# Kernel optimization log

Hardware: AMD Instinct MI355X
Metric: run time of the kernel (lower is better)

## Reference

```python
import jax, jax.numpy as jnp
import numpy as np

D_MODEL = 768
NUM_HEADS = 12
D_K = D_MODEL // NUM_HEADS
D_FF = 3072
EPS = 1e-5


def _layer_norm(x, gamma, beta):
    mu = jnp.mean(x, axis=-1, keepdims=True)
    var = jnp.mean(jnp.square(x - mu), axis=-1, keepdims=True)
    return (x - mu) * jax.lax.rsqrt(var + EPS) * gamma + beta


def setup_inputs() -> dict:
    key = jax.random.key(0)
    ks = jax.random.split(key, 16)
    s = 1.0 / np.sqrt(D_MODEL)
    sf = 1.0 / np.sqrt(D_FF)
    inp = {
        "x": jax.random.normal(ks[0], (2, 2048, D_MODEL), dtype=jnp.float32),
        "Wq": jax.random.uniform(ks[1], (D_MODEL, D_MODEL), jnp.float32, -s, s),
        "bq": jax.random.uniform(ks[2], (D_MODEL,), jnp.float32, -s, s),
        "Wk": jax.random.uniform(ks[3], (D_MODEL, D_MODEL), jnp.float32, -s, s),
        "bk": jax.random.uniform(ks[4], (D_MODEL,), jnp.float32, -s, s),
        "Wv": jax.random.uniform(ks[5], (D_MODEL, D_MODEL), jnp.float32, -s, s),
        "bv": jax.random.uniform(ks[6], (D_MODEL,), jnp.float32, -s, s),
        "Wo": jax.random.uniform(ks[7], (D_MODEL, D_MODEL), jnp.float32, -s, s),
        "bo": jax.random.uniform(ks[8], (D_MODEL,), jnp.float32, -s, s),
        "W1": jax.random.uniform(ks[9], (D_MODEL, D_FF), jnp.float32, -s, s),
        "b1": jax.random.uniform(ks[10], (D_FF,), jnp.float32, -s, s),
        "W2": jax.random.uniform(ks[11], (D_FF, D_MODEL), jnp.float32, -sf, sf),
        "b2": jax.random.uniform(ks[12], (D_MODEL,), jnp.float32, -sf, sf),
        "g1": jnp.ones((D_MODEL,), jnp.float32),
        "be1": jnp.zeros((D_MODEL,), jnp.float32),
        "g2": jnp.ones((D_MODEL,), jnp.float32),
        "be2": jnp.zeros((D_MODEL,), jnp.float32),
    }
    return inp


def reference(x, Wq, bq, Wk, bk, Wv, bv, Wo, bo, W1, b1, W2, b2, g1, be1, g2, be2):
    B, S, _ = x.shape

    def split(h):  # (B,S,D) -> (B,H,S,Dk)
        return h.reshape(B, S, NUM_HEADS, D_K).transpose(0, 2, 1, 3)

    q = split(x @ Wq + bq)
    k = split(x @ Wk + bk)
    v = split(x @ Wv + bv)

    # naive attention: materialize full (B,H,S,S) scores as in the original
    scores = jnp.einsum("bhsd,bhtd->bhst", q, k) / np.sqrt(D_K)
    attn = jax.nn.softmax(scores, axis=-1)
    ctx = jnp.einsum("bhst,bhtd->bhsd", attn, v)
    ctx = ctx.transpose(0, 2, 1, 3).reshape(B, S, D_MODEL)
    attn_out = ctx @ Wo + bo

    x = _layer_norm(x + attn_out, g1, be1)
    ff = jax.nn.relu(x @ W1 + b1) @ W2 + b2
    x = _layer_norm(x + ff, g2, be2)
    return x
```

## Files before the change

kernel.cpp:

```cpp
#include <hip/hip_runtime.h>
#include <cstdint>


typedef unsigned short u16;
typedef unsigned int u32;
typedef __attribute__((ext_vector_type(4))) float f32x4;
typedef __attribute__((ext_vector_type(8))) short s16x8;
typedef __attribute__((ext_vector_type(4))) u16  u16x4;
typedef __attribute__((ext_vector_type(2))) u32  u32x2;

#define AS1 __attribute__((address_space(1)))
#define AS3 __attribute__((address_space(3)))

__device__ __forceinline__ u16 f2b(float f) {
  union { float f; unsigned u; } v; v.f = f;
  unsigned r = v.u + 0x7FFFu + ((v.u >> 16) & 1u);
  return (u16)(r >> 16);
}

__device__ __forceinline__ void gl_lds16(const void* g, void* lds_uniform_base) {
  __builtin_amdgcn_global_load_lds((const AS1 void*)g, (AS3 void*)lds_uniform_base, 16, 0, 0);
}

__device__ __forceinline__ f32x4 mfma16(s16x8 a, s16x8 b, f32x4 c) {
  return __builtin_amdgcn_mfma_f32_16x16x32_bf16(a, b, c, 0, 0, 0);
}

__device__ __forceinline__ u32 cvt_pk_bf16(float lo, float hi) {
  u32 r;
  asm("v_cvt_pk_bf16_f32 %0, %1, %2" : "=v"(r) : "v"(lo), "v"(hi));
  return r;
}

__global__ __launch_bounds__(256) void prep(
    const float* __restrict__ Wq, const float* __restrict__ Wk,
    const float* __restrict__ Wv, const float* __restrict__ Wo,
    const float* __restrict__ W1, const float* __restrict__ W2,
    const float* __restrict__ bq, const float* __restrict__ bk,
    const float* __restrict__ bv, const float* __restrict__ x,
    u16* __restrict__ Wqkv_t, u16* __restrict__ Wo_t,
    u16* __restrict__ W1_t, u16* __restrict__ W2_t,
    float* __restrict__ bqkv, u16* __restrict__ Xb, int convBlocks) {
  __shared__ float ts[32][33];
  const int bid = blockIdx.x;
  const int tx = threadIdx.x, ty = threadIdx.y;
  if (bid < 6912) {
    const float* W; u16* Wt; int K, N, tile;
    if (bid < 2304) {
      int w = bid / 576; tile = bid - w * 576; K = 768; N = 768;
      W = (w == 0) ? Wq : (w == 1) ? Wk : (w == 2) ? Wv : Wo;
      Wt = (w < 3) ? Wqkv_t + (size_t)w * 768 * 768 : Wo_t;
    } else if (bid < 4608) {
      tile = bid - 2304; K = 768; N = 3072; W = W1; Wt = W1_t;
    } else {
      tile = bid - 4608; K = 3072; N = 768; W = W2; Wt = W2_t;
    }
    int ntx = N >> 5;
    int n0 = (tile % ntx) * 32, k0 = (tile / ntx) * 32;
#pragma unroll
    for (int yy = 0; yy < 32; yy += 8)
      ts[ty + yy][tx] = W[(size_t)(k0 + ty + yy) * N + n0 + tx];
    __syncthreads();
#pragma unroll
    for (int yy = 0; yy < 32; yy += 8)
      Wt[(size_t)(n0 + ty + yy) * K + k0 + tx] = f2b(ts[tx][ty + yy]);
  } else if (bid < 6912 + convBlocks) {
    int t = ty * 32 + tx;
    size_t i = ((size_t)(bid - 6912) * 256 + t) * 4;
    f32x4 v = *(const f32x4*)(x + i);
    u16x4 o;
#pragma unroll
    for (int k = 0; k < 4; ++k) o[k] = f2b(v[k]);
    *(u16x4*)(Xb + i) = o;
  } else {
    int t = ty * 32 + tx;
    int i = (bid - 6912 - convBlocks) * 256 + t;
    if (i < 2304) bqkv[i] = (i < 768) ? bq[i] : (i < 1536) ? bk[i - 768] : bv[i - 1536];
  }
}

__global__ __launch_bounds__(256) void transpose_v(const u16* __restrict__ Vh,
                                                   u16* __restrict__ Vt) {
  __shared__ u16 tile[32][33];
  int bh = blockIdx.z;
  int d0 = blockIdx.x * 32, s0 = blockIdx.y * 32;
  const u16* src = Vh + (size_t)bh * 2048 * 64;
  u16* dst = Vt + (size_t)bh * 64 * 2048;
  int x = threadIdx.x, y = threadIdx.y;
#pragma unroll
  for (int yy = 0; yy < 32; yy += 8)
    tile[y + yy][x] = src[(size_t)(s0 + y + yy) * 64 + d0 + x];
  __syncthreads();
#pragma unroll
  for (int yy = 0; yy < 32; yy += 8)
    dst[(size_t)(d0 + y + yy) * 2048 + s0 + x] = tile[x][y + yy];
}

template <int MODE>
__global__ __launch_bounds__(256) void gemm_bt(const u16* __restrict__ A,
                                               const u16* __restrict__ Bt,
                                               const float* __restrict__ bias,
                                               float* __restrict__ Cf, u16* __restrict__ Cb,
                                               u16* __restrict__ Qo, u16* __restrict__ Ko,
                                               u16* __restrict__ Vo, int M, int N, int K,
                                               int Klen) {
  __shared__ __align__(16) u16 lsA[2][128 * 64];
  __shared__ __align__(16) u16 lsB[2][128 * 64];
  const int tid = threadIdx.x;
  const int lane = tid & 63, wave = tid >> 6;
  const int lr = lane & 15, lh = lane >> 4;
  const int wr = wave >> 1, wc = wave & 1;
  const int m0 = blockIdx.y * 128;
  const int n0 = blockIdx.x * 128;
  const int kB = blockIdx.z * Klen;

  f32x4 acc[4][4];
#pragma unroll
  for (int i = 0; i < 4; ++i)
#pragma unroll
    for (int j = 0; j < 4; ++j) acc[i][j] = f32x4{0.f, 0.f, 0.f, 0.f};

  const size_t aBase = (size_t)m0 * K;
  const size_t bBase = (size_t)n0 * K;
  const int srow8 = tid >> 3;
  const int scolE = (((tid & 7) * 16) ^ ((srow8 & 7) << 4)) >> 1;
  const int xk = (lr & 7) << 4;

  auto stage = [&](int buf, int kt) {
#pragma unroll
    for (int i = 0; i < 4; ++i) {
      int row = i * 32 + srow8;
      int ldsOff = buf * 16384 + i * 4096 + wave * 1024;
      gl_lds16(A + aBase + (size_t)row * K + kt + scolE, (char*)lsA + ldsOff);
      gl_lds16(Bt + bBase + (size_t)row * K + kt + scolE, (char*)lsB + ldsOff);
    }
  };

  const int nk = Klen >> 6;
  stage(0, kB);
  for (int t = 0; t < nk; ++t) {
    const int cur = t & 1;
    __syncthreads();
    if (t + 1 < nk) stage(cur ^ 1, kB + (t + 1) * 64);
    const char* baA = (const char*)lsA + cur * 16384;
    const char* baB = (const char*)lsB + cur * 16384;
#pragma unroll
    for (int ks = 0; ks < 2; ++ks) {
      int cb = (ks * 64 + lh * 16) ^ xk;
      s16x8 a[4], b[4];
#pragma unroll
      for (int i = 0; i < 4; ++i) {
        a[i] = *(const s16x8*)(baA + (wr * 64 + i * 16 + lr) * 128 + cb);
        b[i] = *(const s16x8*)(baB + (wc * 64 + i * 16 + lr) * 128 + cb);
      }
#pragma unroll
      for (int i = 0; i < 4; ++i)
#pragma unroll
        for (int j = 0; j < 4; ++j) acc[i][j] = mfma16(a[i], b[j], acc[i][j]);
    }
  }

  float* CfP = Cf + (size_t)blockIdx.z * M * N;
#pragma unroll
  for (int i = 0; i < 4; ++i) {
    int growb = m0 + wr * 64 + i * 16 + lh * 4;
#pragma unroll
    for (int j = 0; j < 4; ++j) {
      int col = n0 + wc * 64 + j * 16 + lr;
      float bv = (MODE != 0 || blockIdx.z == 0) ? bias[col] : 0.f;
#pragma unroll
      for (int q = 0; q < 4; ++q) {
        int grow = growb + q;
        float v = acc[i][j][q] + bv;
        if (MODE == 0) {
          CfP[(size_t)grow * N + col] = v;
        } else if (MODE == 1) {
          Cb[(size_t)grow * N + col] = f2b(fmaxf(v, 0.f));
        } else {
          int sel = col / 768;
          int c2 = col - sel * 768;
          int h = c2 >> 6, d = c2 & 63;
          int b = grow >> 11, s = grow & 2047;
          size_t idx = (((size_t)(b * 12 + h)) * 2048 + s) * 64 + d;
          float vv = (sel == 0) ? v * 0.1803368801f : v;
          u16* dst = (sel == 0) ? Qo : (sel == 1) ? Ko : Vo;
          dst[idx] = f2b(vv);
        }
      }
    }
  }
}

__global__ __launch_bounds__(256, 3) void attn(const u16* __restrict__ Qh,
                                               const u16* __restrict__ Kh,
                                               const u16* __restrict__ Vt,
                                               float* __restrict__ Op,
                                               float* __restrict__ ml,
                                               int nbh, int ntile) {
  __shared__ __align__(16) u16 lsK[2][64 * 64];
  __shared__ __align__(16) u16 lsV[2][64 * 64];
  __shared__ __align__(16) u16 lsP[4][32 * 64];
  const int tid = threadIdx.x, lane = tid & 63, wave = tid >> 6;
  const int lr = lane & 15, lh = lane >> 4;

  int bx = blockIdx.x, bh = blockIdx.y, z = blockIdx.z;
  {
    int total = 16 * nbh * 2;
    if ((total & 7) == 0) {
      int lin = bx + 16 * (bh + nbh * z);
      int nl = (lin & 7) * (total >> 3) + (lin >> 3);
      bx = nl & 15;
      bh = (nl >> 4) % nbh;
      z = nl / (16 * nbh);
    }
  }
  const int q0 = bx * 128 + wave * 32;
  const size_t kvBase = (size_t)bh * 2048 * 64;
  const int tB = z * ntile;

  const int srow = tid >> 3;
  const int scolE = (((tid & 7) * 16) ^ ((srow & 7) << 4)) >> 1;
  const u16* kSrc = Kh + kvBase + (size_t)srow * 64 + scolE;
  const u16* vSrc = Vt + kvBase + (size_t)srow * 2048 + scolE;

  s16x8 qf[2][2];
#pragma unroll
  for (int i = 0; i < 2; ++i)
#pragma unroll
    for (int ks = 0; ks < 2; ++ks)
      qf[i][ks] = *(const s16x8*)(Qh + kvBase + (size_t)(q0 + i * 16 + lr) * 64 +
                                  ks * 32 + lh * 8);

  f32x4 oacc[2][4];
  float mrow[2], lsum[2];
#pragma unroll
  for (int i = 0; i < 2; ++i) {
    mrow[i] = -1e30f; lsum[i] = 0.f;
#pragma unroll
    for (int d = 0; d < 4; ++d) oacc[i][d] = f32x4{0.f, 0.f, 0.f, 0.f};
  }

  auto stageKV = [&](int buf, int t) {
#pragma unroll
    for (int ii = 0; ii < 2; ++ii) {
      int ldsOff = ii * 4096 + wave * 1024;
      gl_lds16(kSrc + (size_t)(t * 64 + ii * 32) * 64, (char*)lsK[buf] + ldsOff);
      gl_lds16(vSrc + (size_t)ii * 32 * 2048 + t * 64, (char*)lsV[buf] + ldsOff);
    }
  };

  stageKV(0, tB);
  for (int it = 0; it < ntile; ++it) {
    const int cur = it & 1;
    __syncthreads();

    s16x8 kb[2][4];
#pragma unroll
    for (int ks = 0; ks < 2; ++ks)
#pragma unroll
      for (int j = 0; j < 4; ++j) {
        int r = j * 16 + lr;
        kb[ks][j] = *(const s16x8*)((const char*)lsK[cur] + r * 128 +
                                    ((ks * 64 + lh * 16) ^ ((r & 7) << 4)));
      }

    if (it + 1 < ntile) stageKV(cur ^ 1, tB + it + 1);

    f32x4 st[2][4];
#pragma unroll
    for (int i = 0; i < 2; ++i)
#pragma unroll
      for (int j = 0; j < 4; ++j) st[i][j] = f32x4{0.f, 0.f, 0.f, 0.f};
    __builtin_amdgcn_s_setprio(1);
#pragma unroll
    for (int ks = 0; ks < 2; ++ks)
#pragma unroll
      for (int j = 0; j < 4; ++j)
#pragma unroll
        for (int i = 0; i < 2; ++i)
          st[i][j] = mfma16(kb[ks][j], qf[i][ks], st[i][j]);
    __builtin_amdgcn_s_setprio(0);

    float mx[2];
    bool need = false;
#pragma unroll
    for (int i = 0; i < 2; ++i) {
      float a0 = fmaxf(fmaxf(st[i][0][0], st[i][0][1]), fmaxf(st[i][0][2], st[i][0][3]));
      float a1 = fmaxf(fmaxf(st[i][1][0], st[i][1][1]), fmaxf(st[i][1][2], st[i][1][3]));
      float a2 = fmaxf(fmaxf(st[i][2][0], st[i][2][1]), fmaxf(st[i][2][2], st[i][2][3]));
      float a3 = fmaxf(fmaxf(st[i][3][0], st[i][3][1]), fmaxf(st[i][3][2], st[i][3][3]));
      float m = fmaxf(fmaxf(a0, a1), fmaxf(a2, a3));
      m = fmaxf(m, __shfl_xor(m, 16));
      m = fmaxf(m, __shfl_xor(m, 32));
      mx[i] = m;
      need = need || (m > mrow[i] + 11.f);
    }
    if (__any(need)) {
#pragma unroll
      for (int i = 0; i < 2; ++i) {
        float mn = fmaxf(mrow[i], mx[i]);
        float al = exp2f(mrow[i] - mn);
        mrow[i] = mn;
        lsum[i] *= al;
#pragma unroll
        for (int d = 0; d < 4; ++d)
#pragma unroll
          for (int q = 0; q < 4; ++q) oacc[i][d][q] *= al;
      }
    }
#pragma unroll
    for (int i = 0; i < 2; ++i) {
      float ps = 0.f;
#pragma unroll
      for (int j = 0; j < 4; ++j) {
        float p0 = exp2f(st[i][j][0] - mrow[i]);
        float p1 = exp2f(st[i][j][1] - mrow[i]);
        float p2 = exp2f(st[i][j][2] - mrow[i]);
        float p3 = exp2f(st[i][j][3] - mrow[i]);
        ps += (p0 + p1) + (p2 + p3);
        u32x2 pk;
        pk.x = cvt_pk_bf16(p0, p1);
        pk.y = cvt_pk_bf16(p2, p3);
        *(u32x2*)((char*)lsP[wave] + (i * 16 + lr) * 128 +
                  ((j * 32 + lh * 8) ^ ((lr & 7) << 4))) = pk;
      }
      ps += __shfl_xor(ps, 16);
      ps += __shfl_xor(ps, 32);
      lsum[i] += ps;
    }

    __builtin_amdgcn_s_setprio(1);
#pragma unroll
    for (int ks = 0; ks < 2; ++ks) {
      s16x8 pa0 = *(const s16x8*)((const char*)lsP[wave] + lr * 128 +
                                  ((ks * 64 + lh * 16) ^ ((lr & 7) << 4)));
      s16x8 pa1 = *(const s16x8*)((const char*)lsP[wave] + (16 + lr) * 128 +
                                  ((ks * 64 + lh * 16) ^ ((lr & 7) << 4)));
#pragma unroll
      for (int d = 0; d < 4; ++d) {
        int r = d * 16 + lr;
        s16x8 vb = *(const s16x8*)((const char*)lsV[cur] + r * 128 +
                                   ((ks * 64 + lh * 16) ^ ((r & 7) << 4)));
        oacc[0][d] = mfma16(vb, pa0, oacc[0][d]);
        oacc[1][d] = mfma16(vb, pa1, oacc[1][d]);
      }
    }
    __builtin_amdgcn_s_setprio(0);
  }

#pragma unroll
  for (int i = 0; i < 2; ++i) {
    int s = q0 + i * 16 + lr;
    size_t r = ((size_t)z * nbh + bh) * 2048 + s;
#pragma unroll
    for (int d = 0; d < 4; ++d)
      *(f32x4*)(Op + r * 64 + d * 16 + lh * 4) = oacc[i][d];
    if (lh == 0) { ml[r * 2] = mrow[i]; ml[r * 2 + 1] = lsum[i]; }
  }
}

__global__ __launch_bounds__(256) void attn_combine(const float* __restrict__ Op,
                                                    const float* __restrict__ ml,
                                                    u16* __restrict__ ctx, int nbh) {
  size_t i = (size_t)blockIdx.x * 256 + threadIdx.x;
  int d4 = (int)(i & 15);
  size_t rs = i >> 4;
  size_t zs = (size_t)nbh * 2048;
  float m0 = ml[rs * 2],        l0 = ml[rs * 2 + 1];
  float m1 = ml[(zs + rs) * 2], l1 = ml[(zs + rs) * 2 + 1];
  float mx = fmaxf(m0, m1);
  float a0 = exp2f(m0 - mx), a1 = exp2f(m1 - mx);
  float inv = 1.f / (l0 * a0 + l1 * a1);
  a0 *= inv; a1 *= inv;
  f32x4 o0 = *(const f32x4*)(Op + rs * 64 + d4 * 4);
  f32x4 o1 = *(const f32x4*)(Op + (zs + rs) * 64 + d4 * 4);
  int bh = (int)(rs >> 11), s = (int)(rs & 2047);
  int b = bh / 12, h = bh - b * 12;
  u16x4 r;
#pragma unroll
  for (int k = 0; k < 4; ++k) r[k] = f2b(o0[k] * a0 + o1[k] * a1);
  *(u16x4*)(ctx + ((size_t)(b * 2048 + s)) * 768 + h * 64 + d4 * 4) = r;
}

template <int NP>
__global__ __launch_bounds__(256) void resid_ln(const float* __restrict__ xin,
                                                const float* __restrict__ yp,
                                                size_t pstride,
                                                const float* __restrict__ gamma,
                                                const float* __restrict__ beta,
                                                float* __restrict__ outf,
                                                u16* __restrict__ outb) {
  const int row = blockIdx.x, t = threadIdx.x;
  const size_t base = (size_t)row * 768;
  float v[3], s = 0.f, s2 = 0.f;
#pragma unroll
  for (int k = 0; k < 3; ++k) {
    int c = t + k * 256;
    float val = xin[base + c];
#pragma unroll
    for (int p = 0; p < NP; ++p) val += yp[p * pstride + base + c];
    v[k] = val; s += val; s2 += val * val;
  }
#pragma unroll
  for (int off = 32; off > 0; off >>= 1) {
    s += __shfl_down(s, off, 64);
    s2 += __shfl_down(s2, off, 64);
  }
  __shared__ float red[8];
  int lane = t & 63, wave = t >> 6;
  if (lane == 0) { red[wave] = s; red[4 + wave] = s2; }
  __syncthreads();
  s = red[0] + red[1] + red[2] + red[3];
  s2 = red[4] + red[5] + red[6] + red[7];
  const float inv = 1.f / 768.f;
  float mu = s * inv;
  float var = fmaxf(s2 * inv - mu * mu, 0.f);
  float rs = rsqrtf(var + 1e-5f);
#pragma unroll
  for (int k = 0; k < 3; ++k) {
    int c = t + k * 256;
    float o = (v[k] - mu) * rs * gamma[c] + beta[c];
    if (outf) outf[base + c] = o;
    if (outb) outb[base + c] = f2b(o);
  }
}

extern "C" void kernel_launch(void* const* d_in, const int* in_sizes, int n_in,
                              void* d_out, int out_size, void* d_ws, size_t ws_size,
                              hipStream_t stream) {
  const float* x   = (const float*)d_in[0];
  const float* Wq  = (const float*)d_in[1];
  const float* bq  = (const float*)d_in[2];
  const float* Wk  = (const float*)d_in[3];
  const float* bk  = (const float*)d_in[4];
  const float* Wv  = (const float*)d_in[5];
  const float* bv  = (const float*)d_in[6];
  const float* Wo  = (const float*)d_in[7];
  const float* bo  = (const float*)d_in[8];
  const float* W1  = (const float*)d_in[9];
  const float* b1  = (const float*)d_in[10];
  const float* W2  = (const float*)d_in[11];
  const float* b2  = (const float*)d_in[12];
  const float* g1  = (const float*)d_in[13];
  const float* be1 = (const float*)d_in[14];
  const float* g2  = (const float*)d_in[15];
  const float* be2 = (const float*)d_in[16];
  float* out = (float*)d_out;

  const int M = in_sizes[0] / 768;
  const int B = M / 2048;
  const int nbh = B * 12;

  char* ws = (char*)d_ws;
  size_t off = 0;
  auto alloc = [&](size_t bytes) -> void* {
    void* p = ws + off;
    off += (bytes + 255) & ~(size_t)255;
    return p;
  };
  u16*   Wqkv_t = (u16*)alloc((size_t)2304 * 768 * 2);
  u16*   Wo_t   = (u16*)alloc((size_t)768 * 768 * 2);
  u16*   W1_t   = (u16*)alloc((size_t)3072 * 768 * 2);
  u16*   W2_t   = (u16*)alloc((size_t)768 * 3072 * 2);
  float* bqkv   = (float*)alloc(2304 * 4);
  u16*   Xb     = (u16*)alloc((size_t)M * 768 * 2);
  u16*   Qh     = (u16*)alloc((size_t)M * 768 * 2);
  u16*   Kh     = (u16*)alloc((size_t)M * 768 * 2);
  u16*   Vh     = (u16*)alloc((size_t)M * 768 * 2);
  u16*   Vt     = (u16*)alloc((size_t)M * 768 * 2);

  size_t opElems = (size_t)2 * nbh * 2048 * 64;
  size_t mlElems = (size_t)2 * nbh * 2048 * 2;
  size_t attnBytes = (opElems + mlElems) * 4;
  size_t pstride = (size_t)M * 768;
  size_t fixedRest = pstride * 4  + pstride * 2  +
                     (size_t)M * 3072 * 2  + 4096;
  size_t need4 = off + ((pstride * 4 * 4 > attnBytes ? pstride * 4 * 4 : attnBytes)) + fixedRest;
  const int SPLIT2 = (ws_size >= need4) ? 4 : 2;
  size_t regionBytes = pstride * 4 * SPLIT2;
  if (regionBytes < attnBytes) regionBytes = attnBytes;
  float* region = (float*)alloc(regionBytes);
  float* Op   = region;
  float* ml   = region + opElems;
  float* ffnPart  = region;
  float* projPart = (float*)Qh;
  float* x1f  = (float*)alloc(pstride * 4);
  u16*   x1b  = (u16*)alloc(pstride * 2);
  u16*   hb   = (u16*)alloc((size_t)M * 3072 * 2);
  u16*   ctx  = Xb;

  dim3 tb(32, 8);
  const int convBlocks = (M * 768) / 1024;
  prep<<<6912 + convBlocks + 9, tb, 0, stream>>>(
      Wq, Wk, Wv, Wo, W1, W2, bq, bk, bv, x,
      Wqkv_t, Wo_t, W1_t, W2_t, bqkv, Xb, convBlocks);

  gemm_bt<2><<<dim3(2304 / 128, M / 128), 256, 0, stream>>>(
      Xb, Wqkv_t, bqkv, nullptr, nullptr, Qh, Kh, Vh, M, 2304, 768, 768);

  transpose_v<<<dim3(2, 64, nbh), tb, 0, stream>>>(Vh, Vt);

  attn<<<dim3(16, nbh, 2), 256, 0, stream>>>(Qh, Kh, Vt, Op, ml, nbh, 16);
  attn_combine<<<nbh * 128, 256, 0, stream>>>(Op, ml, ctx, nbh);

  gemm_bt<0><<<dim3(768 / 128, M / 128, 2), 256, 0, stream>>>(
      ctx, Wo_t, bo, projPart, nullptr, nullptr, nullptr, nullptr, M, 768, 768, 384);

  resid_ln<2><<<M, 256, 0, stream>>>(x, projPart, pstride, g1, be1, x1f, x1b);

  gemm_bt<1><<<dim3(3072 / 128, M / 128), 256, 0, stream>>>(
      x1b, W1_t, b1, nullptr, hb, nullptr, nullptr, nullptr, M, 3072, 768, 768);

  if (SPLIT2 == 4) {
    gemm_bt<0><<<dim3(768 / 128, M / 128, 4), 256, 0, stream>>>(
        hb, W2_t, b2, ffnPart, nullptr, nullptr, nullptr, nullptr, M, 768, 3072, 768);
    resid_ln<4><<<M, 256, 0, stream>>>(x1f, ffnPart, pstride, g2, be2, out, nullptr);
  } else {
    gemm_bt<0><<<dim3(768 / 128, M / 128, 2), 256, 0, stream>>>(
        hb, W2_t, b2, ffnPart, nullptr, nullptr, nullptr, nullptr, M, 768, 3072, 1536);
    resid_ln<2><<<M, 256, 0, stream>>>(x1f, ffnPart, pstride, g2, be2, out, nullptr);
  }
}
```

Measured before the change: 218.8 us.

## Single-buffer LDS in GEMM and attention, prefetch KV via registers, swizzle GEMM grid

The GEMM drops its LDS double buffer and becomes a load, sync, compute, sync loop, and it adds an XCD-aware block index remap. The attention kernel replaces the async global-to-LDS double buffer with a register prefetch of the next K/V tile that is written to a single LDS buffer after compute, and raises its occupancy hint from 3 to 4. The aim is lower LDS use for higher occupancy plus better L2 locality from the remap. The cost is less overlap in the GEMM, where global loads are no longer hidden behind MFMA work, and an extra barrier per tile.

New measurement: 245.1 us. +12.0%, slower.

```diff
diff --git a/kernel.cpp b/kernel.cpp
--- a/kernel.cpp
+++ b/kernel.cpp
@@ -104,15 +104,31 @@
                                                u16* __restrict__ Qo, u16* __restrict__ Ko,
                                                u16* __restrict__ Vo, int M, int N, int K,
                                                int Klen) {
-  __shared__ __align__(16) u16 lsA[2][128 * 64];
-  __shared__ __align__(16) u16 lsB[2][128 * 64];
+  __shared__ __align__(16) u16 lsA[128 * 64];
+  __shared__ __align__(16) u16 lsB[128 * 64];
   const int tid = threadIdx.x;
   const int lane = tid & 63, wave = tid >> 6;
   const int lr = lane & 15, lh = lane >> 4;
   const int wr = wave >> 1, wc = wave & 1;
-  const int m0 = blockIdx.y * 128;
-  const int n0 = blockIdx.x * 128;
-  const int kB = blockIdx.z * Klen;
+
+  int bx, by, bz;
+  {
+    int nx = gridDim.x, ny = gridDim.y, nz = gridDim.z;
+    int total = nx * ny * nz;
+    int lin = blockIdx.x + nx * (blockIdx.y + ny * blockIdx.z);
+    if ((total & 7) == 0) {
+      int key = (lin & 7) * (total >> 3) + (lin >> 3);
+      by = key % ny;
+      int t2 = key / ny;
+      bz = t2 % nz;
+      bx = t2 / nz;
+    } else {
+      bx = blockIdx.x; by = blockIdx.y; bz = blockIdx.z;
+    }
+  }
+  const int m0 = by * 128;
+  const int n0 = bx * 128;
+  const int kB = bz * Klen;
 
   f32x4 acc[4][4];
 #pragma unroll
@@ -126,24 +142,17 @@
   const int scolE = (((tid & 7) * 16) ^ ((srow8 & 7) << 4)) >> 1;
   const int xk = (lr & 7) << 4;
 
-  auto stage = [&](int buf, int kt) {
+  for (int kt = kB; kt < kB + Klen; kt += 64) {
 #pragma unroll
     for (int i = 0; i < 4; ++i) {
       int row = i * 32 + srow8;
-      int ldsOff = buf * 16384 + i * 4096 + wave * 1024;
+      int ldsOff = i * 4096 + wave * 1024;
       gl_lds16(A + aBase + (size_t)row * K + kt + scolE, (char*)lsA + ldsOff);
       gl_lds16(Bt + bBase + (size_t)row * K + kt + scolE, (char*)lsB + ldsOff);
     }
-  };
-
-  const int nk = Klen >> 6;
-  stage(0, kB);
-  for (int t = 0; t < nk; ++t) {
-    const int cur = t & 1;
     __syncthreads();
-    if (t + 1 < nk) stage(cur ^ 1, kB + (t + 1) * 64);
-    const char* baA = (const char*)lsA + cur * 16384;
-    const char* baB = (const char*)lsB + cur * 16384;
+    const char* baA = (const char*)lsA;
+    const char* baB = (const char*)lsB;
 #pragma unroll
     for (int ks = 0; ks < 2; ++ks) {
       int cb = (ks * 64 + lh * 16) ^ xk;
@@ -158,16 +167,17 @@
 #pragma unroll
         for (int j = 0; j < 4; ++j) acc[i][j] = mfma16(a[i], b[j], acc[i][j]);
     }
-  }
-
-  float* CfP = Cf + (size_t)blockIdx.z * M * N;
+    __syncthreads();
+  }
+
+  float* CfP = Cf + (size_t)bz * M * N;
 #pragma unroll
   for (int i = 0; i < 4; ++i) {
     int growb = m0 + wr * 64 + i * 16 + lh * 4;
 #pragma unroll
     for (int j = 0; j < 4; ++j) {
       int col = n0 + wc * 64 + j * 16 + lr;
-      float bv = (MODE != 0 || blockIdx.z == 0) ? bias[col] : 0.f;
+      float bv = (MODE != 0 || bz == 0) ? bias[col] : 0.f;
 #pragma unroll
       for (int q = 0; q < 4; ++q) {
         int grow = growb + q;
@@ -191,14 +201,14 @@
   }
 }
 
-__global__ __launch_bounds__(256, 3) void attn(const u16* __restrict__ Qh,
+__global__ __launch_bounds__(256, 4) void attn(const u16* __restrict__ Qh,
                                                const u16* __restrict__ Kh,
                                                const u16* __restrict__ Vt,
                                                float* __restrict__ Op,
                                                float* __restrict__ ml,
                                                int nbh, int ntile) {
-  __shared__ __align__(16) u16 lsK[2][64 * 64];
-  __shared__ __align__(16) u16 lsV[2][64 * 64];
+  __shared__ __align__(16) u16 lsK[64 * 64];
+  __shared__ __align__(16) u16 lsV[64 * 64];
   __shared__ __align__(16) u16 lsP[4][32 * 64];
   const int tid = threadIdx.x, lane = tid & 63, wave = tid >> 6;
   const int lr = lane & 15, lh = lane >> 4;
@@ -240,19 +250,27 @@
     for (int d = 0; d < 4; ++d) oacc[i][d] = f32x4{0.f, 0.f, 0.f, 0.f};
   }
 
-  auto stageKV = [&](int buf, int t) {
-#pragma unroll
-    for (int ii = 0; ii < 2; ++ii) {
-      int ldsOff = ii * 4096 + wave * 1024;
-      gl_lds16(kSrc + (size_t)(t * 64 + ii * 32) * 64, (char*)lsK[buf] + ldsOff);
-      gl_lds16(vSrc + (size_t)ii * 32 * 2048 + t * 64, (char*)lsV[buf] + ldsOff);
-    }
+  s16x8 kr0, kr1, vr0, vr1;
+  auto loadKV = [&](int t) {
+    kr0 = *(const s16x8*)(kSrc + (size_t)(t * 64) * 64);
+    kr1 = *(const s16x8*)(kSrc + (size_t)(t * 64 + 32) * 64);
+    vr0 = *(const s16x8*)(vSrc + t * 64);
+    vr1 = *(const s16x8*)(vSrc + (size_t)32 * 2048 + t * 64);
   };
-
-  stageKV(0, tB);
+  auto writeKV = [&]() {
+    *(s16x8*)((char*)lsK + tid * 16) = kr0;
+    *(s16x8*)((char*)lsK + 4096 + tid * 16) = kr1;
+    *(s16x8*)((char*)lsV + tid * 16) = vr0;
+    *(s16x8*)((char*)lsV + 4096 + tid * 16) = vr1;
+  };
+
+  loadKV(tB);
+  writeKV();
+  __syncthreads();
+
   for (int it = 0; it < ntile; ++it) {
-    const int cur = it & 1;
-    __syncthreads();
+    const bool more = (it + 1 < ntile);
+    if (more) loadKV(tB + it + 1);
 
     s16x8 kb[2][4];
 #pragma unroll
@@ -260,11 +278,9 @@
 #pragma unroll
       for (int j = 0; j < 4; ++j) {
         int r = j * 16 + lr;
-        kb[ks][j] = *(const s16x8*)((const char*)lsK[cur] + r * 128 +
+        kb[ks][j] = *(const s16x8*)((const char*)lsK + r * 128 +
                                     ((ks * 64 + lh * 16) ^ ((r & 7) << 4)));
       }
-
-    if (it + 1 < ntile) stageKV(cur ^ 1, tB + it + 1);
 
     f32x4 st[2][4];
 #pragma unroll
@@ -339,13 +355,19 @@
 #pragma unroll
       for (int d = 0; d < 4; ++d) {
         int r = d * 16 + lr;
-        s16x8 vb = *(const s16x8*)((const char*)lsV[cur] + r * 128 +
+        s16x8 vb = *(const s16x8*)((const char*)lsV + r * 128 +
                                    ((ks * 64 + lh * 16) ^ ((r & 7) << 4)));
         oacc[0][d] = mfma16(vb, pa0, oacc[0][d]);
         oacc[1][d] = mfma16(vb, pa1, oacc[1][d]);
       }
     }
     __builtin_amdgcn_s_setprio(0);
+
+    __syncthreads();
+    if (more) {
+      writeKV();
+      __syncthreads();
+    }
   }
 
 #pragma unroll
```
